# Optimization experiments

Measured on AMD Instinct MI355X. Metric: run time of the kernel, lower is better.

## Reference

```python
import jax, jax.numpy as jnp
import numpy as np

EMB = 128
N_LIG = 32768
N_REC = 262144
NUM_GRAPHS = 1024
E_LIG = 327680
E_REC = 2097152
LIG_DIMS = [119, 9, 11, 12, 9, 5, 8, 2, 2]
NUM_LAYERS = 3
BN_EPS = 1e-5


def setup_inputs() -> dict:
    key = jax.random.key(0)
    ks = iter(jax.random.split(key, 64))

    lig_x = jnp.stack(
        [jax.random.randint(next(ks), (N_LIG,), 0, d) for d in LIG_DIMS], axis=1
    )  # [N_lig, 9] categorical atom features
    atom_offsets = jnp.asarray(np.cumsum([0] + LIG_DIMS[:-1]), dtype=jnp.int32)
    atom_emb = jax.random.normal(next(ks), (sum(LIG_DIMS), EMB), jnp.float32) * 0.1

    rec_x_int = jax.random.randint(next(ks), (N_REC,), 0, 20)
    rec_x_float = jax.random.normal(next(ks), (N_REC, 199), jnp.float32)
    rec_emb1 = jax.random.normal(next(ks), (20, EMB), jnp.float32) * 0.1
    rec_w = jax.random.normal(next(ks), (199, EMB), jnp.float32) * 0.05
    rec_b = jnp.zeros((EMB,), jnp.float32)

    lig_edge_index = jax.random.randint(next(ks), (2, E_LIG), 0, N_LIG)
    rec_edge_index = jax.random.randint(next(ks), (2, E_REC), 0, N_REC)
    lig_batch = jnp.repeat(jnp.arange(NUM_GRAPHS), N_LIG // NUM_GRAPHS)
    rec_batch = jnp.repeat(jnp.arange(NUM_GRAPHS), N_REC // NUM_GRAPHS)

    def layer_params():
        W = jax.random.normal(next(ks), (NUM_LAYERS, EMB, EMB), jnp.float32) * (1.0 / np.sqrt(EMB))
        b = jnp.zeros((NUM_LAYERS, EMB), jnp.float32)
        gamma = jnp.ones((NUM_LAYERS, EMB), jnp.float32)
        beta = jnp.zeros((NUM_LAYERS, EMB), jnp.float32)
        return W, b, gamma, beta

    lig_W, lig_b, lig_gamma, lig_beta = layer_params()
    rec_W, rec_bc, rec_gamma, rec_beta = layer_params()

    out_w1 = jax.random.normal(next(ks), (2 * EMB, EMB), jnp.float32) * (1.0 / np.sqrt(2 * EMB))
    out_b1 = jnp.zeros((EMB,), jnp.float32)
    out_w2 = jax.random.normal(next(ks), (EMB, 1), jnp.float32) * (1.0 / np.sqrt(EMB))
    out_b2 = jnp.zeros((1,), jnp.float32)

    return dict(
        lig_x=lig_x, rec_x_int=rec_x_int, rec_x_float=rec_x_float,
        lig_edge_index=lig_edge_index, rec_edge_index=rec_edge_index,
        lig_batch=lig_batch, rec_batch=rec_batch, atom_offsets=atom_offsets,
        atom_emb=atom_emb, rec_emb1=rec_emb1, rec_w=rec_w, rec_b=rec_b,
        lig_W=lig_W, lig_b=lig_b, lig_gamma=lig_gamma, lig_beta=lig_beta,
        rec_W=rec_W, rec_bc=rec_bc, rec_gamma=rec_gamma, rec_beta=rec_beta,
        out_w1=out_w1, out_b1=out_b1, out_w2=out_w2, out_b2=out_b2,
    )


def gcn_layer(x, edge_index, W, b, gamma, beta):
    """GCNConv (sym-norm, self loops) -> BatchNorm (batch stats) -> ReLU."""
    n = x.shape[0]
    h = x @ W  # [N, EMB]
    loops = jnp.arange(n)
    src = jnp.concatenate([edge_index[0], loops])
    dst = jnp.concatenate([edge_index[1], loops])
    deg = jax.ops.segment_sum(jnp.ones_like(dst, dtype=h.dtype), dst, num_segments=n)
    dinv = jax.lax.rsqrt(jnp.maximum(deg, 1.0))  # deg >= 1 with self loops
    msg = h[src] * (dinv[src] * dinv[dst])[:, None]  # gather + normalize
    out = jax.ops.segment_sum(msg, dst, num_segments=n) + b
    mu = out.mean(axis=0)
    var = out.var(axis=0)
    out = (out - mu) * jax.lax.rsqrt(var + BN_EPS) * gamma + beta
    return jax.nn.relu(out)


def scatter_mean(x, seg, num_segments):
    s = jax.ops.segment_sum(x, seg, num_segments=num_segments)
    cnt = jax.ops.segment_sum(jnp.ones((x.shape[0],), x.dtype), seg, num_segments=num_segments)
    return s / jnp.maximum(cnt, 1.0)[:, None]


def reference(lig_x, rec_x_int, rec_x_float, lig_edge_index, rec_edge_index,
              lig_batch, rec_batch, atom_offsets, atom_emb, rec_emb1, rec_w, rec_b,
              lig_W, lig_b, lig_gamma, lig_beta, rec_W, rec_bc, rec_gamma, rec_beta,
              out_w1, out_b1, out_w2, out_b2):
    # Node encoders
    lig_h = atom_emb[lig_x + atom_offsets[None, :]].sum(axis=1)        # [N_lig, EMB]
    rec_h = rec_emb1[rec_x_int] + rec_x_float @ rec_w + rec_b          # [N_rec, EMB]

    for l in range(NUM_LAYERS):
        lig_h = gcn_layer(lig_h, lig_edge_index, lig_W[l], lig_b[l], lig_gamma[l], lig_beta[l])
        rec_h = gcn_layer(rec_h, rec_edge_index, rec_W[l], rec_bc[l], rec_gamma[l], rec_beta[l])

    lig_feat = scatter_mean(lig_h, lig_batch, NUM_GRAPHS)
    rec_feat = scatter_mean(rec_h, rec_batch, NUM_GRAPHS)
    z = jnp.concatenate([lig_feat, rec_feat], axis=1)                  # [B, 2*EMB]
    z = jax.nn.relu(z @ out_w1 + out_b1)
    return (z @ out_w2 + out_b2).squeeze(-1)                            # [B]
```

## Files before the change

kernel.cpp:

```cpp
#include <hip/hip_runtime.h>
#include <hip/hip_bf16.h>
#include <cstdint>
#include <cstddef>

#define EMB 128
#define NLIG 32768
#define NREC 262144
#define NGRAPH 1024
#define ELIG 327680
#define EREC 2097152
#define BN_EPS 1e-5f

typedef unsigned short ushort_t;
typedef short bf16x8 __attribute__((ext_vector_type(8)));
typedef float f32x4 __attribute__((ext_vector_type(4)));

__device__ __forceinline__ float bf2f(ushort_t u) {
  union { unsigned int i; float f; } v;
  v.i = ((unsigned int)u) << 16;
  return v.f;
}
__device__ __forceinline__ ushort_t f2bf(float f) {
  __hip_bfloat16 h = __float2bfloat16(f);
  union { __hip_bfloat16 h; ushort_t u; } v;
  v.h = h;
  return v.u;
}


__global__ __launch_bounds__(256)
void gk_count(const int* __restrict__ dst, int* __restrict__ cnt, int E) {
  int e = blockIdx.x * 256 + threadIdx.x;
  if (e < E) atomicAdd(&cnt[dst[e]], 1);
}

__global__ __launch_bounds__(256)
void gk_scan1(const int* __restrict__ cnt, int* __restrict__ off,
              int* __restrict__ bsum, int n) {
  __shared__ int sm[256];
  int t = threadIdx.x;
  int base = blockIdx.x * 1024 + t * 4;
  int v0 = (base + 0 < n) ? cnt[base + 0] : 0;
  int v1 = (base + 1 < n) ? cnt[base + 1] : 0;
  int v2 = (base + 2 < n) ? cnt[base + 2] : 0;
  int v3 = (base + 3 < n) ? cnt[base + 3] : 0;
  int loc = v0 + v1 + v2 + v3;
  sm[t] = loc;
  __syncthreads();
  for (int o = 1; o < 256; o <<= 1) {
    int x = (t >= o) ? sm[t - o] : 0;
    __syncthreads();
    sm[t] += x;
    __syncthreads();
  }
  int run = sm[t] - loc;
  if (base + 0 < n) off[base + 0] = run;
  run += v0;
  if (base + 1 < n) off[base + 1] = run;
  run += v1;
  if (base + 2 < n) off[base + 2] = run;
  run += v2;
  if (base + 3 < n) off[base + 3] = run;
  if (t == 255) bsum[blockIdx.x] = sm[255];
}

__global__ __launch_bounds__(256)
void gk_scan2(int* __restrict__ bsum, int nb) {
  __shared__ int sm[256];
  int t = threadIdx.x;
  int v = (t < nb) ? bsum[t] : 0;
  sm[t] = v;
  __syncthreads();
  for (int o = 1; o < 256; o <<= 1) {
    int x = (t >= o) ? sm[t - o] : 0;
    __syncthreads();
    sm[t] += x;
    __syncthreads();
  }
  if (t < nb) bsum[t] = sm[t] - v;
}

__global__ __launch_bounds__(256)
void gk_scan3(int* __restrict__ off, const int* __restrict__ bsum, int n, int E) {
  int i = blockIdx.x * 256 + threadIdx.x;
  if (i < n) off[i] += bsum[i >> 10];
  if (i == 0) off[n] = E;
}

__global__ __launch_bounds__(256)
void gk_copy(int* __restrict__ d, const int* __restrict__ s, int n) {
  int i = blockIdx.x * 256 + threadIdx.x;
  if (i < n) d[i] = s[i];
}

__global__ __launch_bounds__(256)
void gk_fill(const int* __restrict__ src, const int* __restrict__ dst,
             int* __restrict__ cur, int* __restrict__ csr, int E) {
  int e = blockIdx.x * 256 + threadIdx.x;
  if (e < E) {
    int d = dst[e];
    int pos = atomicAdd(&cur[d], 1);
    csr[pos] = src[e];
  }
}

__global__ __launch_bounds__(256)
void gk_dinv(const int* __restrict__ off, float* __restrict__ dinv, int n) {
  int i = blockIdx.x * 256 + threadIdx.x;
  if (i < n) dinv[i] = rsqrtf((float)(off[i + 1] - off[i] + 1));
}


__global__ __launch_bounds__(128)
void gk_ligenc(const int* __restrict__ lig_x, const int* __restrict__ offs,
               const float* __restrict__ emb, ushort_t* __restrict__ A) {
  __shared__ int idx[9];
  int i = blockIdx.x;
  int c = threadIdx.x;
  if (c < 9) idx[c] = lig_x[i * 9 + c] + offs[c];
  __syncthreads();
  float acc = 0.f;
#pragma unroll
  for (int f = 0; f < 9; ++f) acc += emb[(size_t)idx[f] * EMB + c];
  A[(size_t)i * EMB + c] = f2bf(acc);
}

__global__ __launch_bounds__(256)
void gk_recw2(const float* __restrict__ W, ushort_t* __restrict__ Wt) {
  int idx = blockIdx.x * 256 + threadIdx.x;
  if (idx < 128 * 224) {
    int c = idx / 224, k = idx - c * 224;
    Wt[idx] = (k < 199) ? f2bf(W[(size_t)k * 128 + c]) : (ushort_t)0;
  }
}

__global__ __launch_bounds__(256)
void gk_xcast(const float* __restrict__ X, ushort_t* __restrict__ Xb) {
  const int ITEMS = NREC * 25;
  int stride = gridDim.x * 256;
  for (int v = blockIdx.x * 256 + threadIdx.x; v < ITEMS; v += stride) {
    int row = v / 25, sub = v - row * 25;
    int k0 = sub * 8;
    const float* xr = X + (size_t)row * 199 + k0;
    ushort_t tmp[8];
#pragma unroll
    for (int j = 0; j < 8; ++j) {
      float f = (k0 + j < 199) ? xr[j] : 0.f;
      tmp[j] = f2bf(f);
    }
    *(uint4*)(Xb + (size_t)row * 200 + k0) = *(uint4*)tmp;
  }
}

__global__ __launch_bounds__(256)
void gk_recenc2(const ushort_t* __restrict__ Xb, const int* __restrict__ xi,
                const float* __restrict__ emb1, const ushort_t* __restrict__ Wt,
                const float* __restrict__ b, ushort_t* __restrict__ A) {
  int t = threadIdx.x;
  int row0 = blockIdx.x * 128;
  int w = t >> 6, lane = t & 63;
  int m = lane & 15, quad = lane >> 4;
  int rbase = w * 32;
  int rA = row0 + rbase + m;
  int rB = rA + 16;

  f32x4 acc[2][8];
#pragma unroll
  for (int rt = 0; rt < 2; ++rt)
#pragma unroll
    for (int ct = 0; ct < 8; ++ct) acc[rt][ct] = (f32x4){0.f, 0.f, 0.f, 0.f};

  const ushort_t* xpA = Xb + (size_t)rA * 200 + quad * 8;
  const ushort_t* xpB = Xb + (size_t)rB * 200 + quad * 8;
  const ushort_t* wp = Wt + (size_t)m * 224 + quad * 8;

  for (int ch = 0; ch < 7; ++ch) {
    bf16x8 a0 = *(const bf16x8*)(xpA + ch * 32);
    bf16x8 a1 = *(const bf16x8*)(xpB + ch * 32);
#pragma unroll
    for (int ct = 0; ct < 8; ++ct) {
      bf16x8 bb = *(const bf16x8*)(wp + (size_t)ct * 16 * 224 + ch * 32);
      acc[0][ct] = __builtin_amdgcn_mfma_f32_16x16x32_bf16(a0, bb, acc[0][ct], 0, 0, 0);
      acc[1][ct] = __builtin_amdgcn_mfma_f32_16x16x32_bf16(a1, bb, acc[1][ct], 0, 0, 0);
    }
  }

  float bcol[8];
#pragma unroll
  for (int ct = 0; ct < 8; ++ct) bcol[ct] = b[ct * 16 + m];
#pragma unroll
  for (int rt = 0; rt < 2; ++rt) {
    int rb = row0 + rbase + rt * 16 + quad * 4;
#pragma unroll
    for (int rr = 0; rr < 4; ++rr) {
      int row = rb + rr;
      const float* e = emb1 + (size_t)xi[row] * 128;
#pragma unroll
      for (int ct = 0; ct < 8; ++ct) {
        int c = ct * 16 + m;
        float v = acc[rt][ct][rr] + bcol[ct] + e[c];
        A[(size_t)row * 128 + c] = f2bf(v);
      }
    }
  }
}

__global__ __launch_bounds__(256)
void gk_prep(const float* __restrict__ W, const float* __restrict__ stats,
             const float* __restrict__ gamma, const float* __restrict__ beta,
             float inv_n, int donorm, ushort_t* __restrict__ Wt,
             float* __restrict__ bnscl, float* __restrict__ bnsh) {
  int idx = blockIdx.x * 256 + threadIdx.x;
  if (idx < 128) {
    if (donorm) {
      float mu = stats[idx] * inv_n;
      float var = stats[128 + idx] * inv_n - mu * mu;
      float s = gamma[idx] * rsqrtf(var + BN_EPS);
      bnscl[idx] = s;
      bnsh[idx] = beta[idx] - mu * s;
    } else {
      bnscl[idx] = 1.f;
      bnsh[idx] = 0.f;
    }
  }
  int c = idx >> 7, k = idx & 127;
  Wt[(size_t)c * 128 + k] = f2bf(W[(size_t)k * 128 + c]);
}

__global__ __launch_bounds__(256)
void gk_mm(const ushort_t* __restrict__ Xb, const ushort_t* __restrict__ Wt,
           const float* __restrict__ bnscl, const float* __restrict__ bnsh,
           int donorm, const float* __restrict__ dinv,
           ushort_t* __restrict__ gb) {
  __shared__ ushort_t Xs[128 * 128];
  __shared__ ushort_t Ws[128 * 128];
  int t = threadIdx.x;
  int row0 = blockIdx.x * 128;

  for (int i = t; i < 2048; i += 256) {
    int r = i >> 4, cc = i & 15;
    union { uint4 v; ushort_t s[8]; } u;
    u.v = *(const uint4*)(Xb + (size_t)(row0 + r) * 128 + cc * 8);
    if (donorm) {
#pragma unroll
      for (int j = 0; j < 8; ++j) {
        int k = cc * 8 + j;
        float f = fmaf(bf2f(u.s[j]), bnscl[k], bnsh[k]);
        f = f > 0.f ? f : 0.f;
        u.s[j] = f2bf(f);
      }
    }
    *(uint4*)&Xs[r * 128 + ((cc ^ (r & 15)) * 8)] = u.v;
  }
  for (int i = t; i < 2048; i += 256) {
    int c = i >> 4, cc = i & 15;
    uint4 u = *(const uint4*)(Wt + (size_t)c * 128 + cc * 8);
    *(uint4*)&Ws[c * 128 + ((cc ^ (c & 15)) * 8)] = u;
  }
  __syncthreads();

  int w = t >> 6, lane = t & 63;
  int m = lane & 15, quad = lane >> 4;
  int rbase = w * 32;

  f32x4 acc[2][8];
#pragma unroll
  for (int rt = 0; rt < 2; ++rt)
#pragma unroll
    for (int ct = 0; ct < 8; ++ct) acc[rt][ct] = (f32x4){0.f, 0.f, 0.f, 0.f};

#pragma unroll
  for (int kc8 = 0; kc8 < 16; kc8 += 4) {
    int ck = (kc8 + quad) ^ m;
    bf16x8 a0 = *(const bf16x8*)&Xs[(rbase + m) * 128 + ck * 8];
    bf16x8 a1 = *(const bf16x8*)&Xs[(rbase + 16 + m) * 128 + ck * 8];
#pragma unroll
    for (int ct = 0; ct < 8; ++ct) {
      bf16x8 b = *(const bf16x8*)&Ws[(ct * 16 + m) * 128 + ck * 8];
      acc[0][ct] = __builtin_amdgcn_mfma_f32_16x16x32_bf16(a0, b, acc[0][ct], 0, 0, 0);
      acc[1][ct] = __builtin_amdgcn_mfma_f32_16x16x32_bf16(a1, b, acc[1][ct], 0, 0, 0);
    }
  }

#pragma unroll
  for (int rt = 0; rt < 2; ++rt) {
    int rb = row0 + rbase + rt * 16 + quad * 4;
    float d0 = dinv[rb + 0], d1 = dinv[rb + 1];
    float d2 = dinv[rb + 2], d3 = dinv[rb + 3];
#pragma unroll
    for (int ct = 0; ct < 8; ++ct) {
      int c = ct * 16 + m;
      gb[(size_t)(rb + 0) * 128 + c] = f2bf(acc[rt][ct][0] * d0);
      gb[(size_t)(rb + 1) * 128 + c] = f2bf(acc[rt][ct][1] * d1);
      gb[(size_t)(rb + 2) * 128 + c] = f2bf(acc[rt][ct][2] * d2);
      gb[(size_t)(rb + 3) * 128 + c] = f2bf(acc[rt][ct][3] * d3);
    }
  }
}


__device__ __forceinline__ void gather8(const ushort_t* __restrict__ g, int c0,
                                        int idxv, int q, unsigned int* v) {
#pragma unroll
  for (int k = 0; k < 8; ++k) {
    int idx = __shfl(idxv, q * 8 + k);
    v[k] = *(const unsigned int*)(g + (size_t)idx * 128 + c0);
  }
}

__device__ __forceinline__ void consume8(float2& acc, const unsigned int* v,
                                         int q, int deg) {
#pragma unroll
  for (int k = 0; k < 8; ++k) {
    float m = (q * 8 + k < deg) ? 1.f : 0.f;
    acc.x = fmaf(bf2f((ushort_t)(v[k] & 0xffffu)), m, acc.x);
    acc.y = fmaf(bf2f((ushort_t)(v[k] >> 16)), m, acc.y);
  }
}

__global__ __launch_bounds__(256)
void gk_agg(const ushort_t* __restrict__ g, const int* __restrict__ off,
            const int* __restrict__ csr, const float* __restrict__ dinv,
            ushort_t* __restrict__ outb, float* __restrict__ stats) {
  __shared__ float ls[128];
  __shared__ float lss[128];
  int t = threadIdx.x;
  int slot = t >> 6;
  int lane = t & 63;
  int c0 = lane * 2;
  int i0 = blockIdx.x * 32;

  if (t < 128) { ls[t] = 0.f; lss[t] = 0.f; }
  __syncthreads();

  int offv = off[i0 + min(lane, 32)];

  int idxA[4], idxB[4], dAs[4], dBs[4];
#pragma unroll
  for (int p = 0; p < 4; ++p) {
    int base = slot * 2 + p * 8;
    int eA  = __shfl(offv, base + 0);
    int eB  = __shfl(offv, base + 1);
    int eB1 = __shfl(offv, base + 2);
    dAs[p] = eB - eA;
    dBs[p] = eB1 - eB;
    int adrA = (dAs[p] > 0) ? min(eA + lane, eB - 1) : 0;
    int adrB = (dBs[p] > 0) ? min(eB + lane, eB1 - 1) : 0;
    idxA[p] = csr[adrA];
    idxB[p] = csr[adrB];
  }

  float sx = 0.f, sy = 0.f, ssx = 0.f, ssy = 0.f;

#pragma unroll
  for (int p = 0; p < 4; ++p) {
    int rA = i0 + slot * 2 + p * 8;
    int rB = rA + 1;
    int degA = dAs[p], degB = dBs[p];
    float dA = dinv[rA], dB = dinv[rB];

    unsigned int sU = *(const unsigned int*)(g + (size_t)rA * 128 + c0);
    unsigned int sV = *(const unsigned int*)(g + (size_t)rB * 128 + c0);
    float2 accA = make_float2(bf2f((ushort_t)(sU & 0xffffu)),
                              bf2f((ushort_t)(sU >> 16)));
    float2 accB = make_float2(bf2f((ushort_t)(sV & 0xffffu)),
                              bf2f((ushort_t)(sV >> 16)));

    int dAf = min(degA, 64), dBf = min(degB, 64);
    int nc = (max(dAf, dBf) + 7) >> 3;
    if (nc > 0) {
      unsigned int vA[8], vB[8];
      gather8(g, c0, idxA[p], 0, vA);
      gather8(g, c0, idxB[p], 0, vB);
      for (int q = 1; q < nc; ++q) {
        unsigned int wA[8], wB[8];
        gather8(g, c0, idxA[p], q, wA);
        gather8(g, c0, idxB[p], q, wB);
        consume8(accA, vA, q - 1, dAf);
        consume8(accB, vB, q - 1, dBf);
#pragma unroll
        for (int k = 0; k < 8; ++k) { vA[k] = wA[k]; vB[k] = wB[k]; }
      }
      consume8(accA, vA, nc - 1, dAf);
      consume8(accB, vB, nc - 1, dBf);
    }

    if (degA > 64) {
      int eA = __shfl(offv, slot * 2 + p * 8);
      for (int e = eA + 64; e < eA + degA; ++e) {
        int idx = csr[e];
        unsigned int v = *(const unsigned int*)(g + (size_t)idx * 128 + c0);
        accA.x += bf2f((ushort_t)(v & 0xffffu));
        accA.y += bf2f((ushort_t)(v >> 16));
      }
    }
    if (degB > 64) {
      int eB = __shfl(offv, slot * 2 + p * 8 + 1);
      for (int e = eB + 64; e < eB + degB; ++e) {
        int idx = csr[e];
        unsigned int v = *(const unsigned int*)(g + (size_t)idx * 128 + c0);
        accB.x += bf2f((ushort_t)(v & 0xffffu));
        accB.y += bf2f((ushort_t)(v >> 16));
      }
    }

    accA.x *= dA; accA.y *= dA;
    accB.x *= dB; accB.y *= dB;
    unsigned int oA = (unsigned int)f2bf(accA.x) | ((unsigned int)f2bf(accA.y) << 16);
    unsigned int oB = (unsigned int)f2bf(accB.x) | ((unsigned int)f2bf(accB.y) << 16);
    *(unsigned int*)(outb + (size_t)rA * 128 + c0) = oA;
    *(unsigned int*)(outb + (size_t)rB * 128 + c0) = oB;
    sx += accA.x + accB.x;
    sy += accA.y + accB.y;
    ssx = fmaf(accA.x, accA.x, ssx); ssx = fmaf(accB.x, accB.x, ssx);
    ssy = fmaf(accA.y, accA.y, ssy); ssy = fmaf(accB.y, accB.y, ssy);
  }

  atomicAdd(&ls[c0 + 0], sx);
  atomicAdd(&ls[c0 + 1], sy);
  atomicAdd(&lss[c0 + 0], ssx);
  atomicAdd(&lss[c0 + 1], ssy);
  __syncthreads();
  if (t < 128) {
    atomicAdd(&stats[t], ls[t]);
    atomicAdd(&stats[t + 128], lss[t]);
  }
}

__global__ __launch_bounds__(128)
void gk_pool(const ushort_t* __restrict__ A, const float* __restrict__ stats,
             const float* __restrict__ gamma, const float* __restrict__ beta,
             float inv_n, float* __restrict__ z, int npg, int zoff) {
  int gidx = blockIdx.x;
  int c = threadIdx.x;
  float mu = stats[c] * inv_n;
  float var = stats[128 + c] * inv_n - mu * mu;
  float scl = gamma[c] * rsqrtf(var + BN_EPS);
  float be = beta[c];
  float sum = 0.f;
  int r0 = gidx * npg;
  for (int r = 0; r < npg; ++r) {
    float v = (bf2f(A[(size_t)(r0 + r) * 128 + c]) - mu) * scl + be;
    sum += v > 0.f ? v : 0.f;
  }
  z[(size_t)gidx * 256 + zoff + c] = sum * (1.0f / (float)npg);
}

__global__ __launch_bounds__(128)
void gk_mlp(const float* __restrict__ z, const float* __restrict__ w1,
            const float* __restrict__ b1, const float* __restrict__ w2,
            const float* __restrict__ b2, float* __restrict__ out) {
  __shared__ float zs[256];
  __shared__ float red[128];
  int gidx = blockIdx.x, t = threadIdx.x;
  zs[t] = z[(size_t)gidx * 256 + t];
  zs[t + 128] = z[(size_t)gidx * 256 + 128 + t];
  __syncthreads();
  float acc = b1[t];
  for (int k = 0; k < 256; ++k) acc += zs[k] * w1[(size_t)k * 128 + t];
  acc = (acc > 0.f ? acc : 0.f) * w2[t];
  red[t] = acc;
  __syncthreads();
  for (int o = 64; o > 0; o >>= 1) {
    if (t < o) red[t] += red[t + o];
    __syncthreads();
  }
  if (t == 0) out[gidx] = red[0] + b2[0];
}


extern "C" void kernel_launch(void* const* d_in, const int* in_sizes, int n_in,
                              void* d_out, int out_size, void* d_ws, size_t ws_size,
                              hipStream_t stream) {
  (void)in_sizes; (void)n_in; (void)out_size; (void)ws_size;
  const int*   lig_x       = (const int*)  d_in[0];
  const int*   rec_x_int   = (const int*)  d_in[1];
  const float* rec_x_float = (const float*)d_in[2];
  const int*   lig_ei      = (const int*)  d_in[3];
  const int*   rec_ei      = (const int*)  d_in[4];
  const int*   atom_off    = (const int*)  d_in[7];
  const float* atom_emb    = (const float*)d_in[8];
  const float* rec_emb1    = (const float*)d_in[9];
  const float* rec_w       = (const float*)d_in[10];
  const float* rec_b       = (const float*)d_in[11];
  const float* lig_W       = (const float*)d_in[12];
  const float* lig_gamma   = (const float*)d_in[14];
  const float* lig_beta    = (const float*)d_in[15];
  const float* rec_W       = (const float*)d_in[16];
  const float* rec_gamma   = (const float*)d_in[18];
  const float* rec_beta    = (const float*)d_in[19];
  const float* out_w1      = (const float*)d_in[20];
  const float* out_b1      = (const float*)d_in[21];
  const float* out_w2      = (const float*)d_in[22];
  const float* out_b2      = (const float*)d_in[23];
  float* out = (float*)d_out;

  char* p = (char*)d_ws;
  auto alloc = [&](size_t bytes) -> void* {
    void* r = p;
    p += (bytes + 255) & ~(size_t)255;
    return r;
  };
  ushort_t* Ab     = (ushort_t*)alloc((size_t)NREC * EMB * 2);
  ushort_t* Gb     = (ushort_t*)alloc((size_t)NREC * EMB * 2);
  ushort_t* Wtb    = (ushort_t*)alloc((size_t)EMB * EMB * 2);
  ushort_t* WtK    = (ushort_t*)alloc((size_t)EMB * 224 * 2);
  ushort_t* Xb2    = (ushort_t*)alloc(((size_t)NREC * 200 + 64) * 2);
  float* bnscl     = (float*)alloc(128 * 4);
  float* bnsh      = (float*)alloc(128 * 4);
  float* dinv_lig  = (float*)alloc((size_t)NLIG * 4);
  float* dinv_rec  = (float*)alloc((size_t)NREC * 4);
  int*   cnt_lig   = (int*)  alloc((size_t)NLIG * 4);
  int*   cnt_rec   = (int*)  alloc((size_t)NREC * 4);
  int*   off_lig   = (int*)  alloc((size_t)(NLIG + 8) * 4);
  int*   off_rec   = (int*)  alloc((size_t)(NREC + 8) * 4);
  int*   csr_lig   = (int*)  alloc((size_t)ELIG * 4);
  int*   csr_rec   = (int*)  alloc((size_t)EREC * 4);
  int*   bsum_lig  = (int*)  alloc(256 * 4);
  int*   bsum_rec  = (int*)  alloc(256 * 4);
  float* stats     = (float*)alloc(256 * 4);
  float* z         = (float*)alloc((size_t)NGRAPH * 256 * 4);

  hipMemsetAsync(cnt_lig, 0, (size_t)NLIG * 4, stream);
  hipMemsetAsync(cnt_rec, 0, (size_t)NREC * 4, stream);
  gk_count<<<ELIG / 256, 256, 0, stream>>>(lig_ei + ELIG, cnt_lig, ELIG);
  gk_count<<<EREC / 256, 256, 0, stream>>>(rec_ei + EREC, cnt_rec, EREC);
  gk_scan1<<<NLIG / 1024, 256, 0, stream>>>(cnt_lig, off_lig, bsum_lig, NLIG);
  gk_scan2<<<1, 256, 0, stream>>>(bsum_lig, NLIG / 1024);
  gk_scan3<<<NLIG / 256, 256, 0, stream>>>(off_lig, bsum_lig, NLIG, ELIG);
  gk_scan1<<<NREC / 1024, 256, 0, stream>>>(cnt_rec, off_rec, bsum_rec, NREC);
  gk_scan2<<<1, 256, 0, stream>>>(bsum_rec, NREC / 1024);
  gk_scan3<<<NREC / 256, 256, 0, stream>>>(off_rec, bsum_rec, NREC, EREC);
  gk_copy<<<NLIG / 256, 256, 0, stream>>>(cnt_lig, off_lig, NLIG);
  gk_copy<<<NREC / 256, 256, 0, stream>>>(cnt_rec, off_rec, NREC);
  gk_fill<<<ELIG / 256, 256, 0, stream>>>(lig_ei, lig_ei + ELIG, cnt_lig, csr_lig, ELIG);
  gk_fill<<<EREC / 256, 256, 0, stream>>>(rec_ei, rec_ei + EREC, cnt_rec, csr_rec, EREC);
  gk_dinv<<<NLIG / 256, 256, 0, stream>>>(off_lig, dinv_lig, NLIG);
  gk_dinv<<<NREC / 256, 256, 0, stream>>>(off_rec, dinv_rec, NREC);

  auto run_entity = [&](const float* Wall, const float* gamma, const float* beta,
                        const int* offv, const int* csrv, const float* dinv,
                        int n, int npg, int zoff) {
    float inv_n = 1.0f / (float)n;
    for (int l = 0; l < 3; ++l) {
      const float* W = Wall + (size_t)l * EMB * EMB;
      const float* gm = (l > 0) ? gamma + (size_t)(l - 1) * EMB : gamma;
      const float* bt = (l > 0) ? beta + (size_t)(l - 1) * EMB : beta;
      gk_prep<<<64, 256, 0, stream>>>(W, stats, gm, bt, inv_n, l > 0 ? 1 : 0,
                                      Wtb, bnscl, bnsh);
      hipMemsetAsync(stats, 0, 256 * 4, stream);
      gk_mm<<<n / 128, 256, 0, stream>>>(Ab, Wtb, bnscl, bnsh, l > 0 ? 1 : 0,
                                         dinv, Gb);
      gk_agg<<<n / 32, 256, 0, stream>>>(Gb, offv, csrv, dinv, Ab, stats);
    }
    gk_pool<<<NGRAPH, 128, 0, stream>>>(Ab, stats, gamma + 2 * EMB, beta + 2 * EMB,
                                        inv_n, z, npg, zoff);
  };

  gk_ligenc<<<NLIG, 128, 0, stream>>>(lig_x, atom_off, atom_emb, Ab);
  run_entity(lig_W, lig_gamma, lig_beta, off_lig, csr_lig, dinv_lig,
             NLIG, NLIG / NGRAPH, 0);

  gk_recw2<<<112, 256, 0, stream>>>(rec_w, WtK);
  gk_xcast<<<2048, 256, 0, stream>>>(rec_x_float, Xb2);
  gk_recenc2<<<NREC / 128, 256, 0, stream>>>(Xb2, rec_x_int, rec_emb1,
                                             WtK, rec_b, Ab);
  run_entity(rec_W, rec_gamma, rec_beta, off_rec, csr_rec, dinv_rec,
             NREC, NREC / NGRAPH, EMB);

  gk_mlp<<<NGRAPH, 128, 0, stream>>>(z, out_w1, out_b1, out_w2, out_b2, out);
}
```

Measured before the change: 1.879 ms.

## Split receptor aggregation into two column-half passes for cache locality

Adds a column-split aggregation kernel that gathers only 64 of the 128 feature columns per launch. The receptor graph is aggregated in two passes, halving each pass's gather working set so more of the random neighbor rows stay in L2/MALL. Each half-warp handles one row, preloading up to 32 neighbor indices and pipelining gathers in chunks of 8. The cost is reading the CSR and offsets twice and issuing narrower 4-byte gathers. The ligand path keeps the original kernel.

New measurement: 2.446 ms. 30.2% more time.

```diff
diff --git a/kernel.cpp b/kernel.cpp
--- a/kernel.cpp
+++ b/kernel.cpp
@@ -424,6 +424,115 @@
   if (t < 128) {
     atomicAdd(&stats[t], ls[t]);
     atomicAdd(&stats[t + 128], lss[t]);
+  }
+}
+
+
+__device__ __forceinline__ void gatherc(const ushort_t* __restrict__ g, int c,
+                                        int idxv, int q, int hbase,
+                                        unsigned int* v) {
+#pragma unroll
+  for (int k = 0; k < 8; ++k) {
+    int idx = __shfl(idxv, hbase + q * 8 + k);
+    v[k] = *(const unsigned int*)(g + (size_t)idx * 128 + c);
+  }
+}
+
+__device__ __forceinline__ void consumec(float& ax, float& ay,
+                                         const unsigned int* v, int q, int dc) {
+#pragma unroll
+  for (int k = 0; k < 8; ++k) {
+    float m = (q * 8 + k < dc) ? 1.f : 0.f;
+    ax = fmaf(bf2f((ushort_t)(v[k] & 0xffffu)), m, ax);
+    ay = fmaf(bf2f((ushort_t)(v[k] >> 16)), m, ay);
+  }
+}
+
+__global__ __launch_bounds__(256)
+void gk_aggc(const ushort_t* __restrict__ g, const int* __restrict__ off,
+             const int* __restrict__ csr, const float* __restrict__ dinv,
+             ushort_t* __restrict__ outb, float* __restrict__ stats, int col0) {
+  __shared__ float ls[64];
+  __shared__ float lss[64];
+  int t = threadIdx.x;
+  int w = t >> 6, lane = t & 63;
+  int h = lane >> 5, sl = lane & 31;
+  int hbase = h * 32;
+  int c = col0 + sl * 2;
+  int i0 = blockIdx.x * 32;
+
+  if (t < 64) { ls[t] = 0.f; lss[t] = 0.f; }
+  __syncthreads();
+
+  int offv = off[i0 + min(lane, 32)];
+
+  int idxP[4], degS[4], eS[4], ncw[4];
+#pragma unroll
+  for (int p = 0; p < 4; ++p) {
+    int rb = w * 8 + 2 * p;
+    int eA  = __shfl(offv, rb);
+    int eM  = __shfl(offv, rb + 1);
+    int eB1 = __shfl(offv, rb + 2);
+    int dA = eM - eA, dB = eB1 - eM;
+    ncw[p] = (min(max(dA, dB), 32) + 7) >> 3;
+    int d = h ? dB : dA;
+    int e0 = h ? eM : eA;
+    degS[p] = d;
+    eS[p] = e0;
+    int adr = (d > 0) ? (e0 + min(sl, d - 1)) : 0;
+    idxP[p] = csr[adr];
+  }
+
+  float sx = 0.f, sy = 0.f, ssx = 0.f, ssy = 0.f;
+
+#pragma unroll
+  for (int p = 0; p < 4; ++p) {
+    int row = i0 + w * 8 + 2 * p + h;
+    int d = degS[p];
+    int dc = min(d, 32);
+    float dv = dinv[row];
+    unsigned int su = *(const unsigned int*)(g + (size_t)row * 128 + c);
+    float ax = bf2f((ushort_t)(su & 0xffffu));
+    float ay = bf2f((ushort_t)(su >> 16));
+
+    int nc = ncw[p];
+    if (nc > 0) {
+      unsigned int v[8];
+      gatherc(g, c, idxP[p], 0, hbase, v);
+      for (int q = 1; q < nc; ++q) {
+        unsigned int nv[8];
+        gatherc(g, c, idxP[p], q, hbase, nv);
+        consumec(ax, ay, v, q - 1, dc);
+#pragma unroll
+        for (int k = 0; k < 8; ++k) v[k] = nv[k];
+      }
+      consumec(ax, ay, v, nc - 1, dc);
+    }
+    if (d > 32) {
+      for (int e = eS[p] + 32; e < eS[p] + d; ++e) {
+        int idx = csr[e];
+        unsigned int vv = *(const unsigned int*)(g + (size_t)idx * 128 + c);
+        ax += bf2f((ushort_t)(vv & 0xffffu));
+        ay += bf2f((ushort_t)(vv >> 16));
+      }
+    }
+
+    ax *= dv; ay *= dv;
+    unsigned int o = (unsigned int)f2bf(ax) | ((unsigned int)f2bf(ay) << 16);
+    *(unsigned int*)(outb + (size_t)row * 128 + c) = o;
+    sx += ax; sy += ay;
+    ssx = fmaf(ax, ax, ssx);
+    ssy = fmaf(ay, ay, ssy);
+  }
+
+  atomicAdd(&ls[sl * 2 + 0], sx);
+  atomicAdd(&ls[sl * 2 + 1], sy);
+  atomicAdd(&lss[sl * 2 + 0], ssx);
+  atomicAdd(&lss[sl * 2 + 1], ssy);
+  __syncthreads();
+  if (t < 64) {
+    atomicAdd(&stats[col0 + t], ls[t]);
+    atomicAdd(&stats[128 + col0 + t], lss[t]);
   }
 }
 
@@ -540,7 +649,7 @@
 
   auto run_entity = [&](const float* Wall, const float* gamma, const float* beta,
                         const int* offv, const int* csrv, const float* dinv,
-                        int n, int npg, int zoff) {
+                        int n, int npg, int zoff, int colsplit) {
     float inv_n = 1.0f / (float)n;
     for (int l = 0; l < 3; ++l) {
       const float* W = Wall + (size_t)l * EMB * EMB;
@@ -551,7 +660,12 @@
       hipMemsetAsync(stats, 0, 256 * 4, stream);
       gk_mm<<<n / 128, 256, 0, stream>>>(Ab, Wtb, bnscl, bnsh, l > 0 ? 1 : 0,
                                          dinv, Gb);
-      gk_agg<<<n / 32, 256, 0, stream>>>(Gb, offv, csrv, dinv, Ab, stats);
+      if (colsplit) {
+        gk_aggc<<<n / 32, 256, 0, stream>>>(Gb, offv, csrv, dinv, Ab, stats, 0);
+        gk_aggc<<<n / 32, 256, 0, stream>>>(Gb, offv, csrv, dinv, Ab, stats, 64);
+      } else {
+        gk_agg<<<n / 32, 256, 0, stream>>>(Gb, offv, csrv, dinv, Ab, stats);
+      }
     }
     gk_pool<<<NGRAPH, 128, 0, stream>>>(Ab, stats, gamma + 2 * EMB, beta + 2 * EMB,
                                         inv_n, z, npg, zoff);
@@ -559,14 +673,14 @@
 
   gk_ligenc<<<NLIG, 128, 0, stream>>>(lig_x, atom_off, atom_emb, Ab);
   run_entity(lig_W, lig_gamma, lig_beta, off_lig, csr_lig, dinv_lig,
-             NLIG, NLIG / NGRAPH, 0);
+             NLIG, NLIG / NGRAPH, 0, 0);
 
   gk_recw2<<<112, 256, 0, stream>>>(rec_w, WtK);
   gk_xcast<<<2048, 256, 0, stream>>>(rec_x_float, Xb2);
   gk_recenc2<<<NREC / 128, 256, 0, stream>>>(Xb2, rec_x_int, rec_emb1,
                                              WtK, rec_b, Ab);
   run_entity(rec_W, rec_gamma, rec_beta, off_rec, csr_rec, dinv_rec,
-             NREC, NREC / NGRAPH, EMB);
+             NREC, NREC / NGRAPH, EMB, 1);
 
   gk_mlp<<<NGRAPH, 128, 0, stream>>>(z, out_w1, out_b1, out_w2, out_b2, out);
 }
```

## Batch ligand and receptor pipelines into shared launches per layer

Applied to the files above, without the earlier changes.

Ligand and receptor GCN stages (encoder, weight prep, matmul, aggregation, pooling) are merged into single launches that split the grid by block index, with separate buffers for each entity. The scan kernel also takes over the cursor copy and the degree-inverse computation, removing two kernel pairs. This cuts the launch count and lets the small ligand work fill the GPU alongside receptor blocks rather than running alone. It costs extra memory for separate buffers and adds a branch on block index.

Measured after the change: 1.795 ms. 1.05x faster.

```diff
diff --git a/kernel.cpp b/kernel.cpp
--- a/kernel.cpp
+++ b/kernel.cpp
@@ -81,16 +81,17 @@
 }
 
 __global__ __launch_bounds__(256)
-void gk_scan3(int* __restrict__ off, const int* __restrict__ bsum, int n, int E) {
+void gk_scan3f(int* __restrict__ off, const int* __restrict__ bsum,
+               int* __restrict__ cur, float* __restrict__ dinv, int n, int E) {
   int i = blockIdx.x * 256 + threadIdx.x;
-  if (i < n) off[i] += bsum[i >> 10];
+  if (i < n) {
+    int deg = cur[i];
+    int o = off[i] + bsum[i >> 10];
+    off[i] = o;
+    cur[i] = o;
+    dinv[i] = rsqrtf((float)(deg + 1));
+  }
   if (i == 0) off[n] = E;
-}
-
-__global__ __launch_bounds__(256)
-void gk_copy(int* __restrict__ d, const int* __restrict__ s, int n) {
-  int i = blockIdx.x * 256 + threadIdx.x;
-  if (i < n) d[i] = s[i];
 }
 
 __global__ __launch_bounds__(256)
@@ -104,26 +105,6 @@
   }
 }
 
-__global__ __launch_bounds__(256)
-void gk_dinv(const int* __restrict__ off, float* __restrict__ dinv, int n) {
-  int i = blockIdx.x * 256 + threadIdx.x;
-  if (i < n) dinv[i] = rsqrtf((float)(off[i + 1] - off[i] + 1));
-}
-
-
-__global__ __launch_bounds__(128)
-void gk_ligenc(const int* __restrict__ lig_x, const int* __restrict__ offs,
-               const float* __restrict__ emb, ushort_t* __restrict__ A) {
-  __shared__ int idx[9];
-  int i = blockIdx.x;
-  int c = threadIdx.x;
-  if (c < 9) idx[c] = lig_x[i * 9 + c] + offs[c];
-  __syncthreads();
-  float acc = 0.f;
-#pragma unroll
-  for (int f = 0; f < 9; ++f) acc += emb[(size_t)idx[f] * EMB + c];
-  A[(size_t)i * EMB + c] = f2bf(acc);
-}
 
 __global__ __launch_bounds__(256)
 void gk_recw2(const float* __restrict__ W, ushort_t* __restrict__ Wt) {
@@ -152,12 +133,29 @@
   }
 }
 
-__global__ __launch_bounds__(256)
-void gk_recenc2(const ushort_t* __restrict__ Xb, const int* __restrict__ xi,
-                const float* __restrict__ emb1, const ushort_t* __restrict__ Wt,
-                const float* __restrict__ b, ushort_t* __restrict__ A) {
+#define LIGB (NLIG / 2)
+__global__ __launch_bounds__(256)
+void gk_enc2(const int* __restrict__ lig_x, const int* __restrict__ offs,
+             const float* __restrict__ emb,
+             const ushort_t* __restrict__ Xb, const int* __restrict__ xi,
+             const float* __restrict__ emb1, const ushort_t* __restrict__ Wt,
+             const float* __restrict__ b,
+             ushort_t* __restrict__ Al, ushort_t* __restrict__ Ar) {
   int t = threadIdx.x;
-  int row0 = blockIdx.x * 128;
+  if (blockIdx.x < LIGB) {
+    __shared__ int idx[2][9];
+    int n0 = blockIdx.x * 2;
+    if (t < 9) idx[0][t] = lig_x[n0 * 9 + t] + offs[t];
+    else if (t >= 128 && t < 137) idx[1][t - 128] = lig_x[(n0 + 1) * 9 + (t - 128)] + offs[t - 128];
+    __syncthreads();
+    int half = t >> 7, c = t & 127;
+    float acc = 0.f;
+#pragma unroll
+    for (int f = 0; f < 9; ++f) acc += emb[(size_t)idx[half][f] * EMB + c];
+    Al[(size_t)(n0 + half) * EMB + c] = f2bf(acc);
+    return;
+  }
+  int row0 = (blockIdx.x - LIGB) * 128;
   int w = t >> 6, lane = t & 63;
   int m = lane & 15, quad = lane >> 4;
   int rbase = w * 32;
@@ -199,18 +197,32 @@
       for (int ct = 0; ct < 8; ++ct) {
         int c = ct * 16 + m;
         float v = acc[rt][ct][rr] + bcol[ct] + e[c];
-        A[(size_t)row * 128 + c] = f2bf(v);
+        Ar[(size_t)row * 128 + c] = f2bf(v);
       }
     }
   }
 }
 
 __global__ __launch_bounds__(256)
-void gk_prep(const float* __restrict__ W, const float* __restrict__ stats,
-             const float* __restrict__ gamma, const float* __restrict__ beta,
-             float inv_n, int donorm, ushort_t* __restrict__ Wt,
-             float* __restrict__ bnscl, float* __restrict__ bnsh) {
-  int idx = blockIdx.x * 256 + threadIdx.x;
+void gk_prep2(const float* __restrict__ Wl, const float* __restrict__ Wr,
+              const float* __restrict__ statsAll,
+              const float* __restrict__ gml, const float* __restrict__ btl,
+              const float* __restrict__ gmr, const float* __restrict__ btr,
+              int donorm,
+              ushort_t* __restrict__ Wtl, ushort_t* __restrict__ Wtr,
+              float* __restrict__ scll, float* __restrict__ shl,
+              float* __restrict__ sclr, float* __restrict__ shr) {
+  int bidx = blockIdx.x;
+  bool isl = bidx < 64;
+  const float* W = isl ? Wl : Wr;
+  const float* stats = statsAll + (isl ? 0 : 256);
+  const float* gamma = isl ? gml : gmr;
+  const float* beta = isl ? btl : btr;
+  float inv_n = isl ? (1.f / (float)NLIG) : (1.f / (float)NREC);
+  ushort_t* Wt = isl ? Wtl : Wtr;
+  float* bnscl = isl ? scll : sclr;
+  float* bnsh = isl ? shl : shr;
+  int idx = (isl ? bidx : bidx - 64) * 256 + threadIdx.x;
   if (idx < 128) {
     if (donorm) {
       float mu = stats[idx] * inv_n;
@@ -227,15 +239,27 @@
   Wt[(size_t)c * 128 + k] = f2bf(W[(size_t)k * 128 + c]);
 }
 
-__global__ __launch_bounds__(256)
-void gk_mm(const ushort_t* __restrict__ Xb, const ushort_t* __restrict__ Wt,
-           const float* __restrict__ bnscl, const float* __restrict__ bnsh,
-           int donorm, const float* __restrict__ dinv,
-           ushort_t* __restrict__ gb) {
+#define MMB_L (NLIG / 128)
+__global__ __launch_bounds__(256)
+void gk_mm2(const ushort_t* __restrict__ Xl, const ushort_t* __restrict__ Xr,
+            const ushort_t* __restrict__ Wtl, const ushort_t* __restrict__ Wtr,
+            const float* __restrict__ scll, const float* __restrict__ shl,
+            const float* __restrict__ sclr, const float* __restrict__ shr,
+            int donorm,
+            const float* __restrict__ dinvl, const float* __restrict__ dinvr,
+            ushort_t* __restrict__ gbl, ushort_t* __restrict__ gbr) {
+  bool isl = blockIdx.x < MMB_L;
+  const ushort_t* Xb = isl ? Xl : Xr;
+  const ushort_t* Wt = isl ? Wtl : Wtr;
+  const float* bnscl = isl ? scll : sclr;
+  const float* bnsh = isl ? shl : shr;
+  const float* dinv = isl ? dinvl : dinvr;
+  ushort_t* gb = isl ? gbl : gbr;
+  int row0 = (isl ? blockIdx.x : blockIdx.x - MMB_L) * 128;
+
   __shared__ ushort_t Xs[128 * 128];
   __shared__ ushort_t Ws[128 * 128];
   int t = threadIdx.x;
-  int row0 = blockIdx.x * 128;
 
   for (int i = t; i < 2048; i += 256) {
     int r = i >> 4, cc = i & 15;
@@ -318,17 +342,29 @@
   }
 }
 
-__global__ __launch_bounds__(256)
-void gk_agg(const ushort_t* __restrict__ g, const int* __restrict__ off,
-            const int* __restrict__ csr, const float* __restrict__ dinv,
-            ushort_t* __restrict__ outb, float* __restrict__ stats) {
+#define AGB_L (NLIG / 32)
+__global__ __launch_bounds__(256)
+void gk_agg2(const ushort_t* __restrict__ gl, const ushort_t* __restrict__ gr,
+             const int* __restrict__ offl, const int* __restrict__ offr,
+             const int* __restrict__ csrl, const int* __restrict__ csrr,
+             const float* __restrict__ dinvl, const float* __restrict__ dinvr,
+             ushort_t* __restrict__ outl, ushort_t* __restrict__ outr,
+             float* __restrict__ statsAll) {
+  bool isl = blockIdx.x < AGB_L;
+  const ushort_t* g = isl ? gl : gr;
+  const int* off = isl ? offl : offr;
+  const int* csr = isl ? csrl : csrr;
+  const float* dinv = isl ? dinvl : dinvr;
+  ushort_t* outb = isl ? outl : outr;
+  float* stats = statsAll + (isl ? 0 : 256);
+  int i0 = (isl ? blockIdx.x : blockIdx.x - AGB_L) * 32;
+
   __shared__ float ls[128];
   __shared__ float lss[128];
   int t = threadIdx.x;
   int slot = t >> 6;
   int lane = t & 63;
   int c0 = lane * 2;
-  int i0 = blockIdx.x * 32;
 
   if (t < 128) { ls[t] = 0.f; lss[t] = 0.f; }
   __syncthreads();
@@ -428,10 +464,21 @@
 }
 
 __global__ __launch_bounds__(128)
-void gk_pool(const ushort_t* __restrict__ A, const float* __restrict__ stats,
-             const float* __restrict__ gamma, const float* __restrict__ beta,
-             float inv_n, float* __restrict__ z, int npg, int zoff) {
-  int gidx = blockIdx.x;
+void gk_pool2(const ushort_t* __restrict__ Al, const ushort_t* __restrict__ Ar,
+              const float* __restrict__ statsAll,
+              const float* __restrict__ gml, const float* __restrict__ btl,
+              const float* __restrict__ gmr, const float* __restrict__ btr,
+              float* __restrict__ z) {
+  bool isl = blockIdx.x < NGRAPH;
+  int gidx = isl ? blockIdx.x : blockIdx.x - NGRAPH;
+  const ushort_t* A = isl ? Al : Ar;
+  const float* stats = statsAll + (isl ? 0 : 256);
+  const float* gamma = isl ? gml : gmr;
+  const float* beta = isl ? btl : btr;
+  float inv_n = isl ? (1.f / (float)NLIG) : (1.f / (float)NREC);
+  int npg = isl ? (NLIG / NGRAPH) : (NREC / NGRAPH);
+  int zoff = isl ? 0 : EMB;
+
   int c = threadIdx.x;
   float mu = stats[c] * inv_n;
   float var = stats[128 + c] * inv_n - mu * mu;
@@ -501,13 +548,18 @@
     p += (bytes + 255) & ~(size_t)255;
     return r;
   };
-  ushort_t* Ab     = (ushort_t*)alloc((size_t)NREC * EMB * 2);
-  ushort_t* Gb     = (ushort_t*)alloc((size_t)NREC * EMB * 2);
-  ushort_t* Wtb    = (ushort_t*)alloc((size_t)EMB * EMB * 2);
+  ushort_t* Ab_r   = (ushort_t*)alloc((size_t)NREC * EMB * 2);
+  ushort_t* Gb_r   = (ushort_t*)alloc((size_t)NREC * EMB * 2);
+  ushort_t* Ab_l   = (ushort_t*)alloc((size_t)NLIG * EMB * 2);
+  ushort_t* Gb_l   = (ushort_t*)alloc((size_t)NLIG * EMB * 2);
+  ushort_t* Wtb_l  = (ushort_t*)alloc((size_t)EMB * EMB * 2);
+  ushort_t* Wtb_r  = (ushort_t*)alloc((size_t)EMB * EMB * 2);
   ushort_t* WtK    = (ushort_t*)alloc((size_t)EMB * 224 * 2);
   ushort_t* Xb2    = (ushort_t*)alloc(((size_t)NREC * 200 + 64) * 2);
-  float* bnscl     = (float*)alloc(128 * 4);
-  float* bnsh      = (float*)alloc(128 * 4);
+  float* scl_l     = (float*)alloc(128 * 4);
+  float* sh_l      = (float*)alloc(128 * 4);
+  float* scl_r     = (float*)alloc(128 * 4);
+  float* sh_r      = (float*)alloc(128 * 4);
   float* dinv_lig  = (float*)alloc((size_t)NLIG * 4);
   float* dinv_rec  = (float*)alloc((size_t)NREC * 4);
   int*   cnt_lig   = (int*)  alloc((size_t)NLIG * 4);
@@ -518,7 +570,7 @@
   int*   csr_rec   = (int*)  alloc((size_t)EREC * 4);
   int*   bsum_lig  = (int*)  alloc(256 * 4);
   int*   bsum_rec  = (int*)  alloc(256 * 4);
-  float* stats     = (float*)alloc(256 * 4);
+  float* stats2    = (float*)alloc(512 * 4);
   float* z         = (float*)alloc((size_t)NGRAPH * 256 * 4);
 
   hipMemsetAsync(cnt_lig, 0, (size_t)NLIG * 4, stream);
@@ -527,46 +579,42 @@
   gk_count<<<EREC / 256, 256, 0, stream>>>(rec_ei + EREC, cnt_rec, EREC);
   gk_scan1<<<NLIG / 1024, 256, 0, stream>>>(cnt_lig, off_lig, bsum_lig, NLIG);
   gk_scan2<<<1, 256, 0, stream>>>(bsum_lig, NLIG / 1024);
-  gk_scan3<<<NLIG / 256, 256, 0, stream>>>(off_lig, bsum_lig, NLIG, ELIG);
+  gk_scan3f<<<NLIG / 256, 256, 0, stream>>>(off_lig, bsum_lig, cnt_lig,
+                                            dinv_lig, NLIG, ELIG);
   gk_scan1<<<NREC / 1024, 256, 0, stream>>>(cnt_rec, off_rec, bsum_rec, NREC);
   gk_scan2<<<1, 256, 0, stream>>>(bsum_rec, NREC / 1024);
-  gk_scan3<<<NREC / 256, 256, 0, stream>>>(off_rec, bsum_rec, NREC, EREC);
-  gk_copy<<<NLIG / 256, 256, 0, stream>>>(cnt_lig, off_lig, NLIG);
-  gk_copy<<<NREC / 256, 256, 0, stream>>>(cnt_rec, off_rec, NREC);
+  gk_scan3f<<<NREC / 256, 256, 0, stream>>>(off_rec, bsum_rec, cnt_rec,
+                                            dinv_rec, NREC, EREC);
   gk_fill<<<ELIG / 256, 256, 0, stream>>>(lig_ei, lig_ei + ELIG, cnt_lig, csr_lig, ELIG);
   gk_fill<<<EREC / 256, 256, 0, stream>>>(rec_ei, rec_ei + EREC, cnt_rec, csr_rec, EREC);
-  gk_dinv<<<NLIG / 256, 256, 0, stream>>>(off_lig, dinv_lig, NLIG);
-  gk_dinv<<<NREC / 256, 256, 0, stream>>>(off_rec, dinv_rec, NREC);
-
-  auto run_entity = [&](const float* Wall, const float* gamma, const float* beta,
-                        const int* offv, const int* csrv, const float* dinv,
-                        int n, int npg, int zoff) {
-    float inv_n = 1.0f / (float)n;
-    for (int l = 0; l < 3; ++l) {
-      const float* W = Wall + (size_t)l * EMB * EMB;
-      const float* gm = (l > 0) ? gamma + (size_t)(l - 1) * EMB : gamma;
-      const float* bt = (l > 0) ? beta + (size_t)(l - 1) * EMB : beta;
-      gk_prep<<<64, 256, 0, stream>>>(W, stats, gm, bt, inv_n, l > 0 ? 1 : 0,
-                                      Wtb, bnscl, bnsh);
-      hipMemsetAsync(stats, 0, 256 * 4, stream);
-      gk_mm<<<n / 128, 256, 0, stream>>>(Ab, Wtb, bnscl, bnsh, l > 0 ? 1 : 0,
-                                         dinv, Gb);
-      gk_agg<<<n / 32, 256, 0, stream>>>(Gb, offv, csrv, dinv, Ab, stats);
-    }
-    gk_pool<<<NGRAPH, 128, 0, stream>>>(Ab, stats, gamma + 2 * EMB, beta + 2 * EMB,
-                                        inv_n, z, npg, zoff);
-  };
-
-  gk_ligenc<<<NLIG, 128, 0, stream>>>(lig_x, atom_off, atom_emb, Ab);
-  run_entity(lig_W, lig_gamma, lig_beta, off_lig, csr_lig, dinv_lig,
-             NLIG, NLIG / NGRAPH, 0);
 
   gk_recw2<<<112, 256, 0, stream>>>(rec_w, WtK);
   gk_xcast<<<2048, 256, 0, stream>>>(rec_x_float, Xb2);
-  gk_recenc2<<<NREC / 128, 256, 0, stream>>>(Xb2, rec_x_int, rec_emb1,
-                                             WtK, rec_b, Ab);
-  run_entity(rec_W, rec_gamma, rec_beta, off_rec, csr_rec, dinv_rec,
-             NREC, NREC / NGRAPH, EMB);
-
+  gk_enc2<<<LIGB + NREC / 128, 256, 0, stream>>>(lig_x, atom_off, atom_emb,
+                                                 Xb2, rec_x_int, rec_emb1,
+                                                 WtK, rec_b, Ab_l, Ab_r);
+
+  for (int l = 0; l < 3; ++l) {
+    const float* Wl = lig_W + (size_t)l * EMB * EMB;
+    const float* Wr = rec_W + (size_t)l * EMB * EMB;
+    const float* gml = (l > 0) ? lig_gamma + (size_t)(l - 1) * EMB : lig_gamma;
+    const float* btl = (l > 0) ? lig_beta + (size_t)(l - 1) * EMB : lig_beta;
+    const float* gmr = (l > 0) ? rec_gamma + (size_t)(l - 1) * EMB : rec_gamma;
+    const float* btr = (l > 0) ? rec_beta + (size_t)(l - 1) * EMB : rec_beta;
+    gk_prep2<<<128, 256, 0, stream>>>(Wl, Wr, stats2, gml, btl, gmr, btr,
+                                      l > 0 ? 1 : 0, Wtb_l, Wtb_r,
+                                      scl_l, sh_l, scl_r, sh_r);
+    hipMemsetAsync(stats2, 0, 512 * 4, stream);
+    gk_mm2<<<MMB_L + NREC / 128, 256, 0, stream>>>(
+        Ab_l, Ab_r, Wtb_l, Wtb_r, scl_l, sh_l, scl_r, sh_r, l > 0 ? 1 : 0,
+        dinv_lig, dinv_rec, Gb_l, Gb_r);
+    gk_agg2<<<AGB_L + NREC / 32, 256, 0, stream>>>(
+        Gb_l, Gb_r, off_lig, off_rec, csr_lig, csr_rec,
+        dinv_lig, dinv_rec, Ab_l, Ab_r, stats2);
+  }
+
+  gk_pool2<<<2 * NGRAPH, 128, 0, stream>>>(Ab_l, Ab_r, stats2,
+                                           lig_gamma + 2 * EMB, lig_beta + 2 * EMB,
+                                           rec_gamma + 2 * EMB, rec_beta + 2 * EMB, z);
   gk_mlp<<<NGRAPH, 128, 0, stream>>>(z, out_w1, out_b1, out_w2, out_b2, out);
 }
```
